# Kernel tuning notes

Measured on AMD Instinct MI355X. Metric: run time of the kernel, lower is better.

Reference implementation:

```python
import jax, jax.numpy as jnp
import numpy as np

H = 128; L = 4; N_TOTAL = 2500; M = 4; K = 12
S = N_TOTAL * M          # 10000 subgraphs
F = S * K                # 120000 flat nodes
E_INTRA = 2 * F          # 240000 intra-subgraph edges
E_INTER = 16 * N_TOTAL   # 40000 canonical edges
B = 50; VOCAB = 119; MAX_DIST = 32; BN_EPS = 1e-5


def _bn(x, g, b):
    # training-mode BatchNorm1d over rows (biased var, eps=1e-5)
    mu = x.mean(0)
    var = x.var(0)
    return (x - mu) * jax.lax.rsqrt(var + BN_EPS) * g + b


def _gine(x, ei, ea, W1, b1, W2, b2):
    # PyG GINEConv, eps=0: MLP(x + sum_{src->dst} relu(x[src] + e))
    msg = jax.nn.relu(x[ei[0]] + ea)                              # [E,H]
    agg = jax.ops.segment_sum(msg, ei[1], num_segments=x.shape[0])
    h = x + agg
    return jax.nn.relu(h @ W1 + b1) @ W2 + b2


def setup_inputs():
    key = jax.random.key(0)
    ks = list(jax.random.split(key, 32)); it = iter(ks)
    nk = lambda: next(it)
    rn = lambda shape, s=0.05: jax.random.normal(nk(), shape, dtype=jnp.float32) * s
    x_tok = jax.random.randint(nk(), (F,), 0, VOCAB)
    dist = jax.random.randint(nk(), (F,), 0, MAX_DIST + 1)
    node_ids = jax.random.randint(nk(), (F,), 0, N_TOTAL)
    node_ids = jnp.where(jax.random.uniform(nk(), (F,)) < 0.1, -1, node_ids)
    root_flat_idx = jnp.arange(S) * K
    node_ids = node_ids.at[root_flat_idx].set(jnp.arange(S) // M)  # root = canonical node
    valid = node_ids >= 0
    sub_batch = jnp.repeat(jnp.arange(S), K)
    src = jax.random.randint(nk(), (E_INTRA,), 0, F)
    dst = (src // K) * K + jax.random.randint(nk(), (E_INTRA,), 0, K)  # stay inside subgraph
    intra_ei = jnp.stack([src, dst])
    edge_index = jax.random.randint(nk(), (2, E_INTER), 0, N_TOTAL)
    batch_ids = jnp.arange(N_TOTAL) // (N_TOTAL // B)
    lp = -jax.random.uniform(nk(), (S,)) * 3.0                    # log-probs <= 0
    z = lambda *shape: jnp.zeros(shape, jnp.float32)
    o = lambda *shape: jnp.ones(shape, jnp.float32)
    return dict(
        x_tok=x_tok, dist=dist, node_ids=node_ids, valid=valid,
        sub_batch=sub_batch, root_flat_idx=root_flat_idx,
        intra_ei=intra_ei, edge_index=edge_index, batch_ids=batch_ids,
        lp=lp, ea_flat=rn((E_INTRA, H)), edge_attr=rn((E_INTER, H)),
        atom_emb=rn((VOCAB, H)), dist_emb=rn((MAX_DIST + 1, H)),
        logp_w=rn((1, H)), logp_b=z(H),
        intra_W1=rn((L, H, H)), intra_b1=z(L, H),
        intra_W2=rn((L, H, H)), intra_b2=z(L, H),
        intra_bn_g=o(L, H), intra_bn_b=z(L, H),
        self_W=rn((L, H, H)), self_b=z(L, H),
        root_W=rn((L, H, H)), root_b=z(L, H),
        inter_W1=rn((L, H, H)), inter_b1=z(L, H),
        inter_W2=rn((L, H, H)), inter_b2=z(L, H),
        inter_bn_g=o(L, H), inter_bn_b=z(L, H),
        readout_bn_g=o(H), readout_bn_b=z(H),
        alpha_pool=o(1), alpha_inter=o(1),
    )


def reference(x_tok, dist, node_ids, valid, sub_batch, root_flat_idx, intra_ei,
              edge_index, batch_ids, lp, ea_flat, edge_attr, atom_emb, dist_emb,
              logp_w, logp_b, intra_W1, intra_b1, intra_W2, intra_b2,
              intra_bn_g, intra_bn_b, self_W, self_b, root_W, root_b,
              inter_W1, inter_b1, inter_W2, inter_b2, inter_bn_g, inter_bn_b,
              readout_bn_g, readout_bn_b, alpha_pool, alpha_inter):
    valid_f = valid.astype(jnp.float32)[:, None]                  # [F,1]
    is_root_f = jnp.zeros((F, 1), jnp.float32).at[root_flat_idx].set(1.0)
    clamped_ids = jnp.maximum(node_ids, 0)
    # input encoding: atom embedding + BFS-distance PE + log-prob PE
    logp_pe = jax.nn.relu(lp[sub_batch][:, None] * logp_w[0] + logp_b)
    h = (atom_emb[x_tok] + dist_emb[dist] + logp_pe) * valid_f
    # HT inter-root weights, normalized per canonical root id
    root_ids = node_ids[root_flat_idx]                            # [S]
    rv = root_ids >= 0
    rid = jnp.maximum(root_ids, 0)
    w_un = jnp.where(rv, jnp.exp(-alpha_inter[0] * lp), 0.0)
    w_sum = jax.ops.segment_sum(w_un, rid, num_segments=N_TOTAL)
    ht_w = jnp.where(rv, w_un / (w_sum[rid] + 1e-16), 0.0)        # [S]
    for l in range(L):
        h1 = _gine(h, intra_ei, ea_flat, intra_W1[l], intra_b1[l], intra_W2[l], intra_b2[l])
        h1 = _bn(h1, intra_bn_g[l], intra_bn_b[l]) * valid_f
        h_root_bcast = h[sub_batch * K]
        h_non_root = (h @ self_W[l] + self_b[l]) + (h_root_bcast @ root_W[l] + root_b[l])
        # HT-weighted scatter of root reps to canonical nodes
        h_roots = h[root_flat_idx]                                # [S,H]
        h_root_canon = jax.ops.segment_sum(h_roots * ht_w[:, None], rid, num_segments=N_TOTAL)
        h_inter = _gine(h_root_canon, edge_index, edge_attr, inter_W1[l], inter_b1[l], inter_W2[l], inter_b2[l])
        h_inter = _bn(h_inter, inter_bn_g[l], inter_bn_b[l])
        h_inter_bcast = h_inter[clamped_ids] * valid_f
        out = is_root_f * (h1 + h_inter_bcast) + (1.0 - is_root_f) * (h1 + h_non_root)
        h = jax.nn.relu(out) * valid_f                            # dropout p=0
    # HT softmax readout over the m subgraphs of each canonical node
    h_sub = jax.ops.segment_sum(h * valid_f, sub_batch, num_segments=S)
    h_sub_2d = h_sub.reshape(N_TOTAL, M, H)
    w = jax.nn.softmax(-alpha_pool[0] * lp.reshape(N_TOTAL, M), axis=1)
    node_emb = jnp.einsum('nm,nmh->nh', w, h_sub_2d)
    node_emb = _bn(node_emb, readout_bn_g, readout_bn_b)
    return jax.ops.segment_sum(node_emb, batch_ids, num_segments=B)  # [B,H]
```

## Files before the change

### kernel.cpp

```cpp
#include <hip/hip_runtime.h>
#include <math.h>

#define H 128
#define H4 (H/4)
#define KK 12
#define MSUB 4
#define FF 120000
#define SS 10000
#define NN 2500
#define NBATCH 50
#define NLAYER 4
#define EINTRA 240000
#define EINTER 40000
#define HH (H*H)
#define BN_EPS 1e-5f
#define CAP_I 32
#define CAP_E 96
#define WF_SHORTS 16384
#define ZP 68

typedef short short8 __attribute__((ext_vector_type(8)));
typedef float floatx4 __attribute__((ext_vector_type(4)));

__device__ __forceinline__ unsigned short f2bf_rne(float x){
  unsigned u = __float_as_uint(x);
  unsigned r = u + 0x7FFFu + ((u >> 16) & 1u);
  return (unsigned short)(r >> 16);
}


__global__ void k_zeroi(int* __restrict__ p, int n){
  int i = blockIdx.x*256 + threadIdx.x;
  if (i < n) p[i] = 0;
}


__global__ void k_bucket(const int* __restrict__ dst, int E, int* __restrict__ cnt,
                         int* __restrict__ beid, int cap){
  int e = blockIdx.x*256 + threadIdx.x;
  if (e >= E) return;
  int d = dst[e];
  int p = atomicAdd(&cnt[d], 1);
  if (p < cap) beid[(size_t)d*cap + p] = e;
}

__global__ void k_scan(const int* __restrict__ cnt, int rows, int cap,
                       int* __restrict__ rowptr, int* __restrict__ gcount){
  __shared__ int sdata[256];
  __shared__ int sbase;
  int tid = threadIdx.x;
  int r = blockIdx.x*256 + tid;
  int v = 0;
  if (r < rows){ v = cnt[r]; if (v > cap) v = cap; }
  sdata[tid] = v;
  __syncthreads();
  for (int ofs = 1; ofs < 256; ofs <<= 1){
    int t = (tid >= ofs) ? sdata[tid-ofs] : 0;
    __syncthreads();
    sdata[tid] += t;
    __syncthreads();
  }
  if (tid == 255) sbase = atomicAdd(gcount, sdata[255]);
  __syncthreads();
  if (r < rows) rowptr[r] = sbase + sdata[tid] - v;
}

__global__ void k_csr_fill(const int* __restrict__ cnt, const int* __restrict__ rowptr,
                           const int* __restrict__ beid, const int* __restrict__ src,
                           int rows, int cap, int2* __restrict__ es){
  int f = blockIdx.x*256 + threadIdx.x;
  if (f >= rows) return;
  int n = cnt[f]; if (n > cap) n = cap;
  int base = rowptr[f];
  const int* bl = beid + (size_t)f*cap;
  for (int i = 0; i < n; ++i){
    int e = bl[i];
    es[base + i] = make_int2(e, src[e]);
  }
}


__global__ void k_wprep(const float* __restrict__ iW1, const float* __restrict__ iW2,
                        const float* __restrict__ sW,  const float* __restrict__ rW,
                        const float* __restrict__ nW1, const float* __restrict__ nW2,
                        short* __restrict__ whiG, short* __restrict__ wloG){
  int mat = blockIdx.x >> 3;
  int t = (blockIdx.x & 7)*256 + threadIdx.x;
  int l = t & 63, nt = (t >> 6) & 7, ks = t >> 9;
  int layer = mat / 6, which = mat % 6;
  const float* W;
  switch (which){
    case 0: W = iW1; break; case 1: W = iW2; break; case 2: W = sW; break;
    case 3: W = rW;  break; case 4: W = nW1; break; default: W = nW2; break;
  }
  W += (size_t)layer*HH;
  short* oh = whiG + (size_t)mat*WF_SHORTS;
  short* ol = wloG + (size_t)mat*WF_SHORTS;
  int quad = l >> 4, n15 = l & 15;
  #pragma unroll
  for (int j = 0; j < 8; ++j){
    int k = ks*32 + quad*8 + j;
    int n = nt*16 + n15;
    float v = W[(size_t)k*H + n];
    unsigned short hb = f2bf_rne(v);
    float hf = __uint_as_float((unsigned)hb << 16);
    int idx = (ks*8 + nt)*512 + l*8 + j;
    oh[idx] = (short)hb;
    ol[idx] = (short)f2bf_rne(v - hf);
  }
}


__global__ void k_encode(float* __restrict__ h, const int* __restrict__ xtok,
                         const int* __restrict__ dist, const int* __restrict__ nids,
                         const int* __restrict__ subb, const float* __restrict__ lp,
                         const float* __restrict__ aemb, const float* __restrict__ demb,
                         const float* __restrict__ lw, const float* __restrict__ lb){
  int idx = blockIdx.x*256 + threadIdx.x;
  if (idx >= FF*H4) return;
  int f = idx >> 5; int c = (idx & 31) << 2;
  float vf = (nids[f] >= 0) ? 1.f : 0.f;
  float l = lp[subb[f]];
  float4 a = *(const float4*)(aemb + (size_t)xtok[f]*H + c);
  float4 d = *(const float4*)(demb + (size_t)dist[f]*H + c);
  float4 w = *(const float4*)(lw + c);
  float4 b = *(const float4*)(lb + c);
  float4 o;
  o.x = (a.x + d.x + fmaxf(fmaf(l, w.x, b.x), 0.f)) * vf;
  o.y = (a.y + d.y + fmaxf(fmaf(l, w.y, b.y), 0.f)) * vf;
  o.z = (a.z + d.z + fmaxf(fmaf(l, w.z, b.z), 0.f)) * vf;
  o.w = (a.w + d.w + fmaxf(fmaf(l, w.w, b.w), 0.f)) * vf;
  *(float4*)(h + (size_t)f*H + c) = o;
}


__global__ void k_htw(const int* __restrict__ nids, const int* __restrict__ rfi,
                      const float* __restrict__ lp, const float* __restrict__ alpha,
                      float* __restrict__ htw){
  int n = blockIdx.x*256 + threadIdx.x;
  if (n >= NN) return;
  float a = alpha[0];
  float w[MSUB]; float sum = 0.f;
  #pragma unroll
  for (int m = 0; m < MSUB; ++m){
    int s = n*MSUB + m;
    int rid = nids[rfi[s]];
    float wm = (rid >= 0) ? expf(-a*lp[s]) : 0.f;
    w[m] = wm; sum += wm;
  }
  float inv = 1.f / (sum + 1e-16f);
  #pragma unroll
  for (int m = 0; m < MSUB; ++m) htw[n*MSUB + m] = w[m]*inv;
}


__global__ void k_gine_gather2(float* __restrict__ outa, const float* __restrict__ x,
                               const float* __restrict__ ea, const int* __restrict__ cnt,
                               const int* __restrict__ rowptr, const int2* __restrict__ es,
                               int rows, int cap){
  int idx = blockIdx.x*256 + threadIdx.x;
  if (idx >= rows*H4) return;
  int f = idx >> 5; int c = (idx & 31) << 2;
  float4 acc = *(const float4*)(x + (size_t)f*H + c);
  int n = cnt[f]; if (n > cap) n = cap;
  const int2* p = es + rowptr[f];
  int i = 0;
  for (; i + 2 <= n; i += 2){
    int2 e0 = p[i];
    int2 e1 = p[i+1];
    float4 x0 = *(const float4*)(x + (size_t)e0.y*H + c);
    float4 a0 = *(const float4*)(ea + (size_t)e0.x*H + c);
    float4 x1 = *(const float4*)(x + (size_t)e1.y*H + c);
    float4 a1 = *(const float4*)(ea + (size_t)e1.x*H + c);
    acc.x += fmaxf(x0.x + a0.x, 0.f) + fmaxf(x1.x + a1.x, 0.f);
    acc.y += fmaxf(x0.y + a0.y, 0.f) + fmaxf(x1.y + a1.y, 0.f);
    acc.z += fmaxf(x0.z + a0.z, 0.f) + fmaxf(x1.z + a1.z, 0.f);
    acc.w += fmaxf(x0.w + a0.w, 0.f) + fmaxf(x1.w + a1.w, 0.f);
  }
  if (i < n){
    int2 e0 = p[i];
    float4 x0 = *(const float4*)(x + (size_t)e0.y*H + c);
    float4 a0 = *(const float4*)(ea + (size_t)e0.x*H + c);
    acc.x += fmaxf(x0.x + a0.x, 0.f);
    acc.y += fmaxf(x0.y + a0.y, 0.f);
    acc.z += fmaxf(x0.z + a0.z, 0.f);
    acc.w += fmaxf(x0.w + a0.w, 0.f);
  }
  *(float4*)(outa + (size_t)f*H + c) = acc;
}


__global__ void k_canon(float* __restrict__ canon, const float* __restrict__ h,
                        const float* __restrict__ htw, const int* __restrict__ rfi){
  int idx = blockIdx.x*256 + threadIdx.x;
  if (idx >= NN*H4) return;
  int n = idx >> 5; int c = (idx & 31) << 2;
  float4 acc = make_float4(0.f,0.f,0.f,0.f);
  #pragma unroll
  for (int m = 0; m < MSUB; ++m){
    int s = n*MSUB + m;
    float w = htw[s];
    const float* p = h + (size_t)rfi[s]*H + c;
    acc.x += w*p[0]; acc.y += w*p[1]; acc.z += w*p[2]; acc.w += w*p[3];
  }
  *(float4*)(canon + (size_t)n*H + c) = acc;
}


__device__ __forceinline__ void conv8(const float* av, short8& ah, short8& al){
  #pragma unroll
  for (int j = 0; j < 8; ++j){
    unsigned short hb = f2bf_rne(av[j]);
    float hf = __uint_as_float((unsigned)hb << 16);
    ah[j] = (short)hb;
    al[j] = (short)f2bf_rne(av[j] - hf);
  }
}


__global__ __launch_bounds__(256, 2) void k_mm_mfma(
    const float* __restrict__ in, float* __restrict__ out, int rows,
    const short* __restrict__ whiG, const short* __restrict__ wlo,
    const float* __restrict__ bias, int do_relu, const int* __restrict__ gather)
{
  __shared__ __align__(16) short whi[WF_SHORTS];
  __shared__ __align__(16) float zb[4][16][ZP];
  int tid = threadIdx.x;
  int w = tid >> 6, l = tid & 63;
  int quad = l >> 4, n15 = l & 15;

  #pragma unroll
  for (int i = 0; i < 8; ++i)
    *(short8*)&whi[(tid*8 + i*2048)*1] = *(const short8*)&whiG[(tid + i*256)*8];
  __syncthreads();

  const short* hp = whi + l*8;
  const short* lp = wlo + l*8;
  float (*Z)[ZP] = zb[w];

  int ngroups = (rows + 63) >> 6;
  for (int g = blockIdx.x; g < ngroups; g += gridDim.x){
    int rload = g*64 + w*16 + n15;
    bool okload = rload < rows;
    int ir = okload ? (gather ? gather[rload] : rload) : 0;
    const float* ap = in + (size_t)ir*H + quad*8;

    short8 ah[4], al[4];
    #pragma unroll
    for (int ks = 0; ks < 4; ++ks){
      float4 a0 = okload ? *(const float4*)(ap + ks*32 + 0) : make_float4(0.f,0.f,0.f,0.f);
      float4 a1 = okload ? *(const float4*)(ap + ks*32 + 4) : make_float4(0.f,0.f,0.f,0.f);
      float av[8] = {a0.x,a0.y,a0.z,a0.w,a1.x,a1.y,a1.z,a1.w};
      conv8(av, ah[ks], al[ks]);
    }

    floatx4 acc[8] = {};
    #pragma unroll
    for (int ks = 0; ks < 4; ++ks){
      #pragma unroll
      for (int nt = 0; nt < 8; ++nt){
        short8 bh = *(const short8*)(hp + (ks*8 + nt)*512);
        short8 bl = *(const short8*)(lp + (ks*8 + nt)*512);
        acc[nt] = __builtin_amdgcn_mfma_f32_16x16x32_bf16(ah[ks], bh, acc[nt], 0, 0, 0);
        acc[nt] = __builtin_amdgcn_mfma_f32_16x16x32_bf16(al[ks], bh, acc[nt], 0, 0, 0);
        acc[nt] = __builtin_amdgcn_mfma_f32_16x16x32_bf16(ah[ks], bl, acc[nt], 0, 0, 0);
      }
    }

    int rbase = g*64 + w*16;
    #pragma unroll
    for (int half = 0; half < 2; ++half){
      #pragma unroll
      for (int ntl = 0; ntl < 4; ++ntl){
        int nt = half*4 + ntl;
        float bv = bias[nt*16 + n15];
        #pragma unroll
        for (int reg = 0; reg < 4; ++reg){
          float v = acc[nt][reg] + bv;
          if (do_relu) v = fmaxf(v, 0.f);
          Z[quad*4 + reg][ntl*16 + n15] = v;
        }
      }
      #pragma unroll
      for (int ii = 0; ii < 2; ++ii){
        int row = (l >> 3) + 8*ii;
        int r = rbase + row;
        if (r < rows){
          float* orow = out + (size_t)r*H + half*64;
          #pragma unroll
          for (int jj = 0; jj < 2; ++jj){
            int c4 = ((l & 7) + 8*jj)*4;
            *(float4*)(orow + c4) = *(const float4*)&Z[row][c4];
          }
        }
      }
    }
  }
}


__global__ __launch_bounds__(256, 2) void k_mm_mfma_stats(
    const float* __restrict__ in, float* __restrict__ out, int rows,
    const short* __restrict__ whiG, const short* __restrict__ wlo,
    const float* __restrict__ bias, double* __restrict__ part)
{
  __shared__ __align__(16) short whi[WF_SHORTS];
  __shared__ __align__(16) float zb[4][16][ZP];
  int tid = threadIdx.x;
  int w = tid >> 6, l = tid & 63;
  int quad = l >> 4, n15 = l & 15;

  #pragma unroll
  for (int i = 0; i < 8; ++i)
    *(short8*)&whi[(tid*8 + i*2048)*1] = *(const short8*)&whiG[(tid + i*256)*8];
  __syncthreads();

  const short* hp = whi + l*8;
  const short* lp = wlo + l*8;
  float (*Z)[ZP] = zb[w];

  float s0[8] = {0,0,0,0,0,0,0,0};
  float s1[8] = {0,0,0,0,0,0,0,0};

  int ngroups = (rows + 63) >> 6;
  for (int g = blockIdx.x; g < ngroups; g += gridDim.x){
    int rload = g*64 + w*16 + n15;
    bool okload = rload < rows;
    const float* ap = in + (size_t)(okload ? rload : 0)*H + quad*8;

    short8 ah[4], al[4];
    #pragma unroll
    for (int ks = 0; ks < 4; ++ks){
      float4 a0 = okload ? *(const float4*)(ap + ks*32 + 0) : make_float4(0.f,0.f,0.f,0.f);
      float4 a1 = okload ? *(const float4*)(ap + ks*32 + 4) : make_float4(0.f,0.f,0.f,0.f);
      float av[8] = {a0.x,a0.y,a0.z,a0.w,a1.x,a1.y,a1.z,a1.w};
      conv8(av, ah[ks], al[ks]);
    }

    floatx4 acc[8] = {};
    #pragma unroll
    for (int ks = 0; ks < 4; ++ks){
      #pragma unroll
      for (int nt = 0; nt < 8; ++nt){
        short8 bh = *(const short8*)(hp + (ks*8 + nt)*512);
        short8 bl = *(const short8*)(lp + (ks*8 + nt)*512);
        acc[nt] = __builtin_amdgcn_mfma_f32_16x16x32_bf16(ah[ks], bh, acc[nt], 0, 0, 0);
        acc[nt] = __builtin_amdgcn_mfma_f32_16x16x32_bf16(al[ks], bh, acc[nt], 0, 0, 0);
        acc[nt] = __builtin_amdgcn_mfma_f32_16x16x32_bf16(ah[ks], bl, acc[nt], 0, 0, 0);
      }
    }

    int rbase = g*64 + w*16;
    #pragma unroll
    for (int half = 0; half < 2; ++half){
      #pragma unroll
      for (int ntl = 0; ntl < 4; ++ntl){
        int nt = half*4 + ntl;
        float bv = bias[nt*16 + n15];
        #pragma unroll
        for (int reg = 0; reg < 4; ++reg){
          float v = acc[nt][reg] + bv;
          if (rbase + quad*4 + reg < rows){ s0[nt] += v; s1[nt] += v*v; }
          Z[quad*4 + reg][ntl*16 + n15] = v;
        }
      }
      #pragma unroll
      for (int ii = 0; ii < 2; ++ii){
        int row = (l >> 3) + 8*ii;
        int r = rbase + row;
        if (r < rows){
          float* orow = out + (size_t)r*H + half*64;
          #pragma unroll
          for (int jj = 0; jj < 2; ++jj){
            int c4 = ((l & 7) + 8*jj)*4;
            *(float4*)(orow + c4) = *(const float4*)&Z[row][c4];
          }
        }
      }
    }
  }

  __syncthreads();
  double* red = (double*)&zb[0][0][0];
  #pragma unroll
  for (int nt = 0; nt < 8; ++nt){
    float a = s0[nt], b = s1[nt];
    a += __shfl_xor(a, 16, 64); b += __shfl_xor(b, 16, 64);
    a += __shfl_xor(a, 32, 64); b += __shfl_xor(b, 32, 64);
    if (quad == 0){
      int col = nt*16 + n15;
      red[(size_t)(w*2+0)*H + col] = (double)a;
      red[(size_t)(w*2+1)*H + col] = (double)b;
    }
  }
  __syncthreads();
  if (tid < H){
    int col = tid;
    double a = red[0*H+col] + red[2*H+col] + red[4*H+col] + red[6*H+col];
    double b = red[1*H+col] + red[3*H+col] + red[5*H+col] + red[7*H+col];
    part[(size_t)(blockIdx.x*2+0)*H + col] = a;
    part[(size_t)(blockIdx.x*2+1)*H + col] = b;
  }
}


__global__ void k_bnstats_p(const float* __restrict__ x, int rows, double* __restrict__ part){
  int g = blockIdx.x*256 + threadIdx.x;
  int c = g & (H-1);
  int s = g >> 7;
  int stride = (gridDim.x*256) >> 7;
  double a = 0.0, b = 0.0;
  for (int r = s; r < rows; r += stride){
    float v = x[(size_t)r*H + c];
    a += v; b += (double)v*(double)v;
  }
  part[(size_t)(s*2+0)*H + c] = a;
  part[(size_t)(s*2+1)*H + c] = b;
}

__global__ void k_bnfin_par(const double* __restrict__ part, int nstreams, int rows,
                            float* __restrict__ muinv){
  __shared__ double sh0[256], sh1[256];
  int c = blockIdx.x;
  int tid = threadIdx.x;
  double a = 0.0, b = 0.0;
  for (int s = tid; s < nstreams; s += 256){
    a += part[(size_t)(s*2+0)*H + c];
    b += part[(size_t)(s*2+1)*H + c];
  }
  sh0[tid] = a; sh1[tid] = b;
  __syncthreads();
  for (int ofs = 128; ofs > 0; ofs >>= 1){
    if (tid < ofs){ sh0[tid] += sh0[tid+ofs]; sh1[tid] += sh1[tid+ofs]; }
    __syncthreads();
  }
  if (tid == 0){
    double mu = sh0[0] / (double)rows;
    double var = sh1[0] / (double)rows - mu*mu;
    muinv[c]   = (float)mu;
    muinv[H+c] = (float)(1.0 / sqrt(var + (double)BN_EPS));
  }
}

__global__ void k_bnapply(float* __restrict__ x, const float* __restrict__ muinv,
                          const float* __restrict__ g, const float* __restrict__ b, int rows){
  int idx = blockIdx.x*256 + threadIdx.x;
  if (idx >= rows*H4) return;
  int r = idx >> 5; int c = (idx & 31) << 2;
  float4 v  = *(const float4*)(x + (size_t)r*H + c);
  float4 mu = *(const float4*)(muinv + c);
  float4 iv = *(const float4*)(muinv + H + c);
  float4 gg = *(const float4*)(g + c);
  float4 bb = *(const float4*)(b + c);
  v.x = (v.x-mu.x)*iv.x*gg.x + bb.x;
  v.y = (v.y-mu.y)*iv.y*gg.y + bb.y;
  v.z = (v.z-mu.z)*iv.z*gg.z + bb.z;
  v.w = (v.w-mu.w)*iv.w*gg.w + bb.w;
  *(float4*)(x + (size_t)r*H + c) = v;
}


__global__ void k_combine(float* __restrict__ h, const float* __restrict__ h1raw,
                          const float* __restrict__ r1, const float* __restrict__ r2,
                          const float* __restrict__ hinter, const float* __restrict__ muinv,
                          const float* __restrict__ bg, const float* __restrict__ bb,
                          const int* __restrict__ nids){
  int idx = blockIdx.x*256 + threadIdx.x;
  if (idx >= FF*H4) return;
  int f = idx >> 5; int c = (idx & 31) << 2;
  int nid = nids[f];
  float vf = (nid >= 0) ? 1.f : 0.f;
  int cid = (nid < 0) ? 0 : nid;
  float4 x  = *(const float4*)(h1raw + (size_t)f*H + c);
  float4 mu = *(const float4*)(muinv + c);
  float4 iv = *(const float4*)(muinv + H + c);
  float4 g4 = *(const float4*)(bg + c);
  float4 b4 = *(const float4*)(bb + c);
  float4 h1;
  h1.x = ((x.x-mu.x)*iv.x*g4.x + b4.x) * vf;
  h1.y = ((x.y-mu.y)*iv.y*g4.y + b4.y) * vf;
  h1.z = ((x.z-mu.z)*iv.z*g4.z + b4.z) * vf;
  h1.w = ((x.w-mu.w)*iv.w*g4.w + b4.w) * vf;
  float4 o;
  if (f % KK == 0){
    float4 hi = *(const float4*)(hinter + (size_t)cid*H + c);
    o.x = h1.x + hi.x*vf; o.y = h1.y + hi.y*vf; o.z = h1.z + hi.z*vf; o.w = h1.w + hi.w*vf;
  } else {
    float4 a  = *(const float4*)(r1 + (size_t)f*H + c);
    float4 rr = *(const float4*)(r2 + (size_t)(f/KK)*H + c);
    o.x = h1.x + a.x + rr.x; o.y = h1.y + a.y + rr.y; o.z = h1.z + a.z + rr.z; o.w = h1.w + a.w + rr.w;
  }
  o.x = fmaxf(o.x,0.f)*vf; o.y = fmaxf(o.y,0.f)*vf; o.z = fmaxf(o.z,0.f)*vf; o.w = fmaxf(o.w,0.f)*vf;
  *(float4*)(h + (size_t)f*H + c) = o;
}


__global__ void k_hsub(float* __restrict__ hsub, const float* __restrict__ h){
  int idx = blockIdx.x*256 + threadIdx.x;
  if (idx >= SS*H4) return;
  int s = idx >> 5; int c = (idx & 31) << 2;
  float4 acc = make_float4(0.f,0.f,0.f,0.f);
  const float* base = h + (size_t)s*KK*H + c;
  #pragma unroll
  for (int k = 0; k < KK; ++k){
    float4 v = *(const float4*)(base + (size_t)k*H);
    acc.x += v.x; acc.y += v.y; acc.z += v.z; acc.w += v.w;
  }
  *(float4*)(hsub + (size_t)s*H + c) = acc;
}

__global__ void k_poolw(float* __restrict__ poolw, const float* __restrict__ lp,
                        const float* __restrict__ alpha){
  int n = blockIdx.x*256 + threadIdx.x;
  if (n >= NN) return;
  float a = alpha[0];
  float s0 = -a*lp[n*MSUB+0], s1 = -a*lp[n*MSUB+1], s2 = -a*lp[n*MSUB+2], s3 = -a*lp[n*MSUB+3];
  float m = fmaxf(fmaxf(s0,s1), fmaxf(s2,s3));
  float e0 = expf(s0-m), e1 = expf(s1-m), e2 = expf(s2-m), e3 = expf(s3-m);
  float sum = e0+e1+e2+e3;
  poolw[n*MSUB+0] = e0/sum; poolw[n*MSUB+1] = e1/sum;
  poolw[n*MSUB+2] = e2/sum; poolw[n*MSUB+3] = e3/sum;
}

__global__ void k_nodeemb(float* __restrict__ nemb, const float* __restrict__ hsub,
                          const float* __restrict__ poolw){
  int idx = blockIdx.x*256 + threadIdx.x;
  if (idx >= NN*H4) return;
  int n = idx >> 5; int c = (idx & 31) << 2;
  float w0 = poolw[n*MSUB+0], w1 = poolw[n*MSUB+1], w2 = poolw[n*MSUB+2], w3 = poolw[n*MSUB+3];
  const float* base = hsub + (size_t)n*MSUB*H + c;
  float4 v0 = *(const float4*)(base + 0*H);
  float4 v1 = *(const float4*)(base + 1*H);
  float4 v2 = *(const float4*)(base + 2*H);
  float4 v3 = *(const float4*)(base + 3*H);
  float4 o;
  o.x = w0*v0.x + w1*v1.x + w2*v2.x + w3*v3.x;
  o.y = w0*v0.y + w1*v1.y + w2*v2.y + w3*v3.y;
  o.z = w0*v0.z + w1*v1.z + w2*v2.z + w3*v3.z;
  o.w = w0*v0.w + w1*v1.w + w2*v2.w + w3*v3.w;
  *(float4*)(nemb + (size_t)n*H + c) = o;
}

__global__ void k_out(float* __restrict__ out, const float* __restrict__ nemb,
                      const float* __restrict__ muinv, const float* __restrict__ g,
                      const float* __restrict__ b){
  int idx = blockIdx.x*256 + threadIdx.x;
  if (idx >= NBATCH*H) return;
  int bi = idx >> 7; int c = idx & (H-1);
  float mu = muinv[c], iv = muinv[H+c], gg = g[c], bb = b[c];
  float acc = 0.f;
  const float* base = nemb + (size_t)bi*(NN/NBATCH)*H + c;
  for (int i = 0; i < NN/NBATCH; ++i)
    acc += (base[(size_t)i*H] - mu)*iv*gg + bb;
  out[idx] = acc;
}


extern "C" void kernel_launch(void* const* d_in, const int* in_sizes, int n_in,
                              void* d_out, int out_size, void* d_ws, size_t ws_size,
                              hipStream_t stream) {
  const int*   x_tok      = (const int*)  d_in[0];
  const int*   dist       = (const int*)  d_in[1];
  const int*   node_ids   = (const int*)  d_in[2];
  const int*   sub_batch  = (const int*)  d_in[4];
  const int*   rfi        = (const int*)  d_in[5];
  const int*   intra_ei   = (const int*)  d_in[6];
  const int*   edge_index = (const int*)  d_in[7];
  const float* lp         = (const float*)d_in[9];
  const float* ea_flat    = (const float*)d_in[10];
  const float* edge_attr  = (const float*)d_in[11];
  const float* atom_emb   = (const float*)d_in[12];
  const float* dist_emb   = (const float*)d_in[13];
  const float* logp_w     = (const float*)d_in[14];
  const float* logp_b     = (const float*)d_in[15];
  const float* intra_W1   = (const float*)d_in[16];
  const float* intra_b1   = (const float*)d_in[17];
  const float* intra_W2   = (const float*)d_in[18];
  const float* intra_b2   = (const float*)d_in[19];
  const float* intra_bn_g = (const float*)d_in[20];
  const float* intra_bn_b = (const float*)d_in[21];
  const float* self_W     = (const float*)d_in[22];
  const float* self_b     = (const float*)d_in[23];
  const float* root_W     = (const float*)d_in[24];
  const float* root_b     = (const float*)d_in[25];
  const float* inter_W1   = (const float*)d_in[26];
  const float* inter_b1   = (const float*)d_in[27];
  const float* inter_W2   = (const float*)d_in[28];
  const float* inter_b2   = (const float*)d_in[29];
  const float* inter_bn_g = (const float*)d_in[30];
  const float* inter_bn_b = (const float*)d_in[31];
  const float* ro_bn_g    = (const float*)d_in[32];
  const float* ro_bn_b    = (const float*)d_in[33];
  const float* alpha_pool = (const float*)d_in[34];
  const float* alpha_inter= (const float*)d_in[35];

  const int* isrc = intra_ei;
  const int* idst = intra_ei + EINTRA;
  const int* esrc = edge_index;
  const int* edst = edge_index + EINTER;

  float* out = (float*)d_out;

  char* ws = (char*)d_ws;
  size_t off = 0;
  auto nxt = [&](size_t bytes) -> void* {
    void* p = ws + off;
    off += (bytes + 255) & ~(size_t)255;
    return p;
  };
  const int G_MM_F = 768;
  const int G_MM_S = (SS + 63)/64;
  const int G_MM_N = (NN + 63)/64;
  const int G_BN_S = 32;

  float*  h      = (float*) nxt((size_t)FF*H*4);
  float*  hmid   = (float*) nxt((size_t)FF*H*4);
  float*  tbuf   = (float*) nxt((size_t)FF*H*4);
  float*  r2     = (float*) nxt((size_t)SS*H*4);
  float*  canon  = (float*) nxt((size_t)NN*H*4);
  float*  agg2   = (float*) nxt((size_t)NN*H*4);
  float*  hsub   = (float*) nxt((size_t)SS*H*4);
  float*  nemb   = (float*) nxt((size_t)NN*H*4);
  float*  htw    = (float*) nxt((size_t)SS*4);
  float*  poolw  = (float*) nxt((size_t)NN*MSUB*4);
  double* statsA = (double*)nxt((size_t)G_MM_F*2*H*8);
  double* statsB = (double*)nxt((size_t)(G_BN_S*2)*2*H*8);
  float*  muinvA = (float*) nxt((size_t)2*H*4);
  float*  muinvB = (float*) nxt((size_t)2*H*4);
  short*  whiG   = (short*) nxt((size_t)24*WF_SHORTS*2);
  short*  wloG   = (short*) nxt((size_t)24*WF_SHORTS*2);
  int*    icnt   = (int*)   nxt((size_t)FF*4);
  int*    ibeid  = (int*)   nxt((size_t)FF*CAP_I*4);
  int*    ecnt   = (int*)   nxt((size_t)NN*4);
  int*    ebeid  = (int*)   nxt((size_t)NN*CAP_E*4);
  int*    irow   = (int*)   nxt((size_t)FF*4);
  int*    erow   = (int*)   nxt((size_t)NN*4);
  int2*   ies    = (int2*)  nxt((size_t)EINTRA*8);
  int2*   ees    = (int2*)  nxt((size_t)EINTER*8);
  int*    gcnt   = (int*)   nxt((size_t)2*4);
  (void)ws_size; (void)n_in; (void)in_sizes; (void)out_size; (void)sub_batch;

  const int G_FH4 = FF*H4/256;
  const int G_SH4 = SS*H4/256;
  const int G_NH4 = (NN*H4 + 255)/256;
  const int G_N   = (NN + 255)/256;
  const int G_F   = (FF + 255)/256;

  k_zeroi<<<G_F, 256, 0, stream>>>(icnt, FF);
  k_zeroi<<<G_N, 256, 0, stream>>>(ecnt, NN);
  k_zeroi<<<1, 256, 0, stream>>>(gcnt, 2);

  k_wprep<<<24*8, 256, 0, stream>>>(intra_W1, intra_W2, self_W, root_W,
                                    inter_W1, inter_W2, whiG, wloG);

  k_bucket<<<(EINTRA+255)/256, 256, 0, stream>>>(idst, EINTRA, icnt, ibeid, CAP_I);
  k_bucket<<<(EINTER+255)/256, 256, 0, stream>>>(edst, EINTER, ecnt, ebeid, CAP_E);
  k_scan<<<G_F, 256, 0, stream>>>(icnt, FF, CAP_I, irow, gcnt);
  k_scan<<<G_N, 256, 0, stream>>>(ecnt, NN, CAP_E, erow, gcnt+1);
  k_csr_fill<<<G_F, 256, 0, stream>>>(icnt, irow, ibeid, isrc, FF, CAP_I, ies);
  k_csr_fill<<<G_N, 256, 0, stream>>>(ecnt, erow, ebeid, esrc, NN, CAP_E, ees);

  k_encode<<<G_FH4, 256, 0, stream>>>(h, x_tok, dist, node_ids, sub_batch, lp,
                                      atom_emb, dist_emb, logp_w, logp_b);
  k_htw<<<G_N, 256, 0, stream>>>(node_ids, rfi, lp, alpha_inter, htw);

  for (int l = 0; l < NLAYER; ++l){
    const short* hi_iW1 = whiG + (size_t)(l*6+0)*WF_SHORTS;
    const short* hi_iW2 = whiG + (size_t)(l*6+1)*WF_SHORTS;
    const short* hi_sW  = whiG + (size_t)(l*6+2)*WF_SHORTS;
    const short* hi_rW  = whiG + (size_t)(l*6+3)*WF_SHORTS;
    const short* hi_nW1 = whiG + (size_t)(l*6+4)*WF_SHORTS;
    const short* hi_nW2 = whiG + (size_t)(l*6+5)*WF_SHORTS;
    const short* lo_iW1 = wloG + (size_t)(l*6+0)*WF_SHORTS;
    const short* lo_iW2 = wloG + (size_t)(l*6+1)*WF_SHORTS;
    const short* lo_sW  = wloG + (size_t)(l*6+2)*WF_SHORTS;
    const short* lo_rW  = wloG + (size_t)(l*6+3)*WF_SHORTS;
    const short* lo_nW1 = wloG + (size_t)(l*6+4)*WF_SHORTS;
    const short* lo_nW2 = wloG + (size_t)(l*6+5)*WF_SHORTS;

    k_gine_gather2<<<G_FH4, 256, 0, stream>>>(hmid, h, ea_flat, icnt, irow, ies, FF, CAP_I);
    k_mm_mfma<<<G_MM_F, 256, 0, stream>>>(hmid, tbuf, FF, hi_iW1, lo_iW1,
                                          intra_b1 + (size_t)l*H, 1, nullptr);
    k_mm_mfma_stats<<<G_MM_F, 256, 0, stream>>>(tbuf, hmid, FF, hi_iW2, lo_iW2,
                                                intra_b2 + (size_t)l*H, statsA);
    k_bnfin_par<<<H, 256, 0, stream>>>(statsA, G_MM_F, FF, muinvA);

    k_canon<<<G_NH4, 256, 0, stream>>>(canon, h, htw, rfi);
    k_mm_mfma<<<G_MM_S, 256, 0, stream>>>(h, r2, SS, hi_rW, lo_rW,
                                          root_b + (size_t)l*H, 0, rfi);

    k_gine_gather2<<<G_NH4, 256, 0, stream>>>(agg2, canon, edge_attr, ecnt, erow, ees, NN, CAP_E);
    k_mm_mfma<<<G_MM_N, 256, 0, stream>>>(agg2, tbuf, NN, hi_nW1, lo_nW1,
                                          inter_b1 + (size_t)l*H, 1, nullptr);
    k_mm_mfma<<<G_MM_N, 256, 0, stream>>>(tbuf, agg2, NN, hi_nW2, lo_nW2,
                                          inter_b2 + (size_t)l*H, 0, nullptr);
    k_bnstats_p<<<G_BN_S, 256, 0, stream>>>(agg2, NN, statsB);
    k_bnfin_par<<<H, 256, 0, stream>>>(statsB, G_BN_S*2, NN, muinvB);
    k_bnapply<<<G_NH4, 256, 0, stream>>>(agg2, muinvB, inter_bn_g + (size_t)l*H,
                                         inter_bn_b + (size_t)l*H, NN);

    k_mm_mfma<<<G_MM_F, 256, 0, stream>>>(h, tbuf, FF, hi_sW, lo_sW,
                                          self_b + (size_t)l*H, 0, nullptr);
    k_combine<<<G_FH4, 256, 0, stream>>>(h, hmid, tbuf, r2, agg2, muinvA,
                                         intra_bn_g + (size_t)l*H,
                                         intra_bn_b + (size_t)l*H, node_ids);
  }

  k_hsub<<<G_SH4, 256, 0, stream>>>(hsub, h);
  k_poolw<<<G_N, 256, 0, stream>>>(poolw, lp, alpha_pool);
  k_nodeemb<<<G_NH4, 256, 0, stream>>>(nemb, hsub, poolw);
  k_bnstats_p<<<G_BN_S, 256, 0, stream>>>(nemb, NN, statsB);
  k_bnfin_par<<<H, 256, 0, stream>>>(statsB, G_BN_S*2, NN, muinvB);
  k_out<<<(NBATCH*H+255)/256, 256, 0, stream>>>(out, nemb, muinvB, ro_bn_g, ro_bn_b);
}
```

Measured before the change: 2.066 ms.

## Stage low weight fragments in LDS, prefetch next A tile, store directly

The MFMA GEMM kernels now copy both the hi and lo bf16 weight fragments into shared memory, where previously the lo half was read from global memory. The main GEMM software-pipelines its grid-stride loop by loading the next row group's A tile into registers while the current tile is multiplied. Both kernels drop the LDS staging buffer for the epilogue and write each result element straight to global memory, which gives narrower, less coalesced stores. The flat-row grid shrinks from 768 to 512 blocks, and the larger LDS footprint and the extra prefetch registers may lower occupancy.

```diff
diff --git a/kernel.cpp b/kernel.cpp
--- a/kernel.cpp
+++ b/kernel.cpp
@@ -17,7 +17,6 @@
 #define CAP_I 32
 #define CAP_E 96
 #define WF_SHORTS 16384
-#define ZP 68
 
 typedef short short8 __attribute__((ext_vector_type(8)));
 typedef float floatx4 __attribute__((ext_vector_type(4)));
@@ -207,52 +206,67 @@
 }
 
 
-__device__ __forceinline__ void conv8(const float* av, short8& ah, short8& al){
+__device__ __forceinline__ void load_a_raw(const float* __restrict__ in, int rows, int rload,
+                                           const int* __restrict__ gather, int quad, float4* ra){
+  bool ok = rload < rows;
+  int ir = ok ? (gather ? gather[rload] : rload) : 0;
+  const float* ap = in + (size_t)ir*H + quad*8;
   #pragma unroll
-  for (int j = 0; j < 8; ++j){
-    unsigned short hb = f2bf_rne(av[j]);
-    float hf = __uint_as_float((unsigned)hb << 16);
-    ah[j] = (short)hb;
-    al[j] = (short)f2bf_rne(av[j] - hf);
+  for (int ks = 0; ks < 4; ++ks){
+    ra[ks*2+0] = ok ? *(const float4*)(ap + ks*32 + 0) : make_float4(0.f,0.f,0.f,0.f);
+    ra[ks*2+1] = ok ? *(const float4*)(ap + ks*32 + 4) : make_float4(0.f,0.f,0.f,0.f);
+  }
+}
+
+__device__ __forceinline__ void conv_a(const float4* ra, short8* ah, short8* al){
+  #pragma unroll
+  for (int ks = 0; ks < 4; ++ks){
+    float av[8] = {ra[ks*2].x, ra[ks*2].y, ra[ks*2].z, ra[ks*2].w,
+                   ra[ks*2+1].x, ra[ks*2+1].y, ra[ks*2+1].z, ra[ks*2+1].w};
+    #pragma unroll
+    for (int j = 0; j < 8; ++j){
+      unsigned short hb = f2bf_rne(av[j]);
+      float hf = __uint_as_float((unsigned)hb << 16);
+      ah[ks][j] = (short)hb;
+      al[ks][j] = (short)f2bf_rne(av[j] - hf);
+    }
   }
 }
 
 
 __global__ __launch_bounds__(256, 2) void k_mm_mfma(
     const float* __restrict__ in, float* __restrict__ out, int rows,
-    const short* __restrict__ whiG, const short* __restrict__ wlo,
+    const short* __restrict__ whiG, const short* __restrict__ wloG,
     const float* __restrict__ bias, int do_relu, const int* __restrict__ gather)
 {
-  __shared__ __align__(16) short whi[WF_SHORTS];
-  __shared__ __align__(16) float zb[4][16][ZP];
+  __shared__ __align__(16) short wfrag[2*WF_SHORTS];
   int tid = threadIdx.x;
   int w = tid >> 6, l = tid & 63;
   int quad = l >> 4, n15 = l & 15;
 
-  #pragma unroll
-  for (int i = 0; i < 8; ++i)
-    *(short8*)&whi[(tid*8 + i*2048)*1] = *(const short8*)&whiG[(tid + i*256)*8];
+  {
+    short8* wdst = (short8*)wfrag;
+    const short8* hs = (const short8*)whiG;
+    const short8* ls = (const short8*)wloG;
+    #pragma unroll
+    for (int i = 0; i < 8; ++i) wdst[tid + i*256] = hs[tid + i*256];
+    #pragma unroll
+    for (int i = 0; i < 8; ++i) wdst[2048 + tid + i*256] = ls[tid + i*256];
+  }
   __syncthreads();
 
-  const short* hp = whi + l*8;
-  const short* lp = wlo + l*8;
-  float (*Z)[ZP] = zb[w];
+  const short* hp = wfrag + l*8;
+  const short* lp = wfrag + WF_SHORTS + l*8;
 
   int ngroups = (rows + 63) >> 6;
-  for (int g = blockIdx.x; g < ngroups; g += gridDim.x){
-    int rload = g*64 + w*16 + n15;
-    bool okload = rload < rows;
-    int ir = okload ? (gather ? gather[rload] : rload) : 0;
-    const float* ap = in + (size_t)ir*H + quad*8;
-
+  int g = blockIdx.x;
+  float4 ra[8];
+  if (g < ngroups) load_a_raw(in, rows, g*64 + w*16 + n15, gather, quad, ra);
+  while (g < ngroups){
+    int gn = g + gridDim.x;
     short8 ah[4], al[4];
-    #pragma unroll
-    for (int ks = 0; ks < 4; ++ks){
-      float4 a0 = okload ? *(const float4*)(ap + ks*32 + 0) : make_float4(0.f,0.f,0.f,0.f);
-      float4 a1 = okload ? *(const float4*)(ap + ks*32 + 4) : make_float4(0.f,0.f,0.f,0.f);
-      float av[8] = {a0.x,a0.y,a0.z,a0.w,a1.x,a1.y,a1.z,a1.w};
-      conv8(av, ah[ks], al[ks]);
-    }
+    conv_a(ra, ah, al);
+    if (gn < ngroups) load_a_raw(in, rows, gn*64 + w*16 + n15, gather, quad, ra);
 
     floatx4 acc[8] = {};
     #pragma unroll
@@ -267,57 +281,49 @@
       }
     }
 
-    int rbase = g*64 + w*16;
-    #pragma unroll
-    for (int half = 0; half < 2; ++half){
+    int rbase = g*64 + w*16 + quad*4;
+    #pragma unroll
+    for (int nt = 0; nt < 8; ++nt){
+      int col = nt*16 + n15;
+      float bv = bias[col];
       #pragma unroll
-      for (int ntl = 0; ntl < 4; ++ntl){
-        int nt = half*4 + ntl;
-        float bv = bias[nt*16 + n15];
-        #pragma unroll
-        for (int reg = 0; reg < 4; ++reg){
+      for (int reg = 0; reg < 4; ++reg){
+        int r = rbase + reg;
+        if (r < rows){
           float v = acc[nt][reg] + bv;
           if (do_relu) v = fmaxf(v, 0.f);
-          Z[quad*4 + reg][ntl*16 + n15] = v;
-        }
-      }
-      #pragma unroll
-      for (int ii = 0; ii < 2; ++ii){
-        int row = (l >> 3) + 8*ii;
-        int r = rbase + row;
-        if (r < rows){
-          float* orow = out + (size_t)r*H + half*64;
-          #pragma unroll
-          for (int jj = 0; jj < 2; ++jj){
-            int c4 = ((l & 7) + 8*jj)*4;
-            *(float4*)(orow + c4) = *(const float4*)&Z[row][c4];
-          }
+          out[(size_t)r*H + col] = v;
         }
       }
     }
+    g = gn;
   }
 }
 
 
 __global__ __launch_bounds__(256, 2) void k_mm_mfma_stats(
     const float* __restrict__ in, float* __restrict__ out, int rows,
-    const short* __restrict__ whiG, const short* __restrict__ wlo,
+    const short* __restrict__ whiG, const short* __restrict__ wloG,
     const float* __restrict__ bias, double* __restrict__ part)
 {
-  __shared__ __align__(16) short whi[WF_SHORTS];
-  __shared__ __align__(16) float zb[4][16][ZP];
+  __shared__ __align__(16) short wfrag[2*WF_SHORTS];
   int tid = threadIdx.x;
   int w = tid >> 6, l = tid & 63;
   int quad = l >> 4, n15 = l & 15;
 
-  #pragma unroll
-  for (int i = 0; i < 8; ++i)
-    *(short8*)&whi[(tid*8 + i*2048)*1] = *(const short8*)&whiG[(tid + i*256)*8];
+  {
+    short8* wdst = (short8*)wfrag;
+    const short8* hs = (const short8*)whiG;
+    const short8* ls = (const short8*)wloG;
+    #pragma unroll
+    for (int i = 0; i < 8; ++i) wdst[tid + i*256] = hs[tid + i*256];
+    #pragma unroll
+    for (int i = 0; i < 8; ++i) wdst[2048 + tid + i*256] = ls[tid + i*256];
+  }
   __syncthreads();
 
-  const short* hp = whi + l*8;
-  const short* lp = wlo + l*8;
-  float (*Z)[ZP] = zb[w];
+  const short* hp = wfrag + l*8;
+  const short* lp = wfrag + WF_SHORTS + l*8;
 
   float s0[8] = {0,0,0,0,0,0,0,0};
   float s1[8] = {0,0,0,0,0,0,0,0};
@@ -334,7 +340,13 @@
       float4 a0 = okload ? *(const float4*)(ap + ks*32 + 0) : make_float4(0.f,0.f,0.f,0.f);
       float4 a1 = okload ? *(const float4*)(ap + ks*32 + 4) : make_float4(0.f,0.f,0.f,0.f);
       float av[8] = {a0.x,a0.y,a0.z,a0.w,a1.x,a1.y,a1.z,a1.w};
-      conv8(av, ah[ks], al[ks]);
+      #pragma unroll
+      for (int j = 0; j < 8; ++j){
+        unsigned short hb = f2bf_rne(av[j]);
+        float hf = __uint_as_float((unsigned)hb << 16);
+        ah[ks][j] = (short)hb;
+        al[ks][j] = (short)f2bf_rne(av[j] - hf);
+      }
     }
 
     floatx4 acc[8] = {};
@@ -350,38 +362,26 @@
       }
     }
 
-    int rbase = g*64 + w*16;
-    #pragma unroll
-    for (int half = 0; half < 2; ++half){
+    int rbase = g*64 + w*16 + quad*4;
+    #pragma unroll
+    for (int nt = 0; nt < 8; ++nt){
+      int col = nt*16 + n15;
+      float bv = bias[col];
       #pragma unroll
-      for (int ntl = 0; ntl < 4; ++ntl){
-        int nt = half*4 + ntl;
-        float bv = bias[nt*16 + n15];
-        #pragma unroll
-        for (int reg = 0; reg < 4; ++reg){
+      for (int reg = 0; reg < 4; ++reg){
+        int r = rbase + reg;
+        if (r < rows){
           float v = acc[nt][reg] + bv;
-          if (rbase + quad*4 + reg < rows){ s0[nt] += v; s1[nt] += v*v; }
-          Z[quad*4 + reg][ntl*16 + n15] = v;
-        }
-      }
-      #pragma unroll
-      for (int ii = 0; ii < 2; ++ii){
-        int row = (l >> 3) + 8*ii;
-        int r = rbase + row;
-        if (r < rows){
-          float* orow = out + (size_t)r*H + half*64;
-          #pragma unroll
-          for (int jj = 0; jj < 2; ++jj){
-            int c4 = ((l & 7) + 8*jj)*4;
-            *(float4*)(orow + c4) = *(const float4*)&Z[row][c4];
-          }
+          out[(size_t)r*H + col] = v;
+          s0[nt] += v;
+          s1[nt] += v*v;
         }
       }
     }
   }
 
   __syncthreads();
-  double* red = (double*)&zb[0][0][0];
+  double* red = (double*)&wfrag[0];
   #pragma unroll
   for (int nt = 0; nt < 8; ++nt){
     float a = s0[nt], b = s1[nt];
@@ -608,7 +608,7 @@
     off += (bytes + 255) & ~(size_t)255;
     return p;
   };
-  const int G_MM_F = 768;
+  const int G_MM_F = 512;
   const int G_MM_S = (SS + 63)/64;
   const int G_MM_N = (NN + 63)/64;
   const int G_BN_S = 32;
```

New measurement: 1.836 ms. 1.13x faster.
